# Kernel tuning notes

Measured on AMD Instinct MI355X. Metric: run time of the kernel, lower is better.

## Reference

```python
import jax, jax.numpy as jnp
import numpy as np

C_LIGHT = 1.0
CHUNK = 363  # 35937 = 99 * 363 spatial modes per scan step


def _spatial_mode_sum(r, spatial_kernel):
    # sum_n spatial_kernel[n] * sin(n * r), reduced over modes in chunks so we
    # never materialize the full [N, 35937] sin table.
    M = spatial_kernel.shape[0]
    nn = jnp.arange(M, dtype=r.dtype).reshape(-1, CHUNK)      # [steps, CHUNK]
    kk = spatial_kernel.reshape(-1, CHUNK)                    # [steps, CHUNK]

    def body(acc, nk):
        n_c, k_c = nk
        # [N, CHUNK] @ [CHUNK] -> [N]
        return acc + jnp.sin(r[:, None] * n_c[None, :]) @ k_c, None

    acc, _ = jax.lax.scan(body, jnp.zeros_like(r), (nn, kk))
    return acc


def setup_inputs() -> dict:
    key = jax.random.key(0)
    k1, k2, k3 = jax.random.split(key, 3)
    N = 131072
    M_SPATIAL = 35937   # (2*16+1)**3
    M_TEMPORAL = 33     # 2*16+1
    return {
        "spacetime_coords": jax.random.normal(k1, (N, 4), jnp.float32) * 2.0,
        "spatial_kernel": jax.random.normal(k2, (M_SPATIAL,), jnp.float32) * 0.1,
        "temporal_kernel": jax.random.normal(k3, (M_TEMPORAL,), jnp.float32) * 0.1,
        "mass_parameter": jnp.float32(1.0),
        "coupling_strength": jnp.float32(0.1),
    }


def reference(spacetime_coords, spatial_kernel, temporal_kernel,
              mass_parameter, coupling_strength):
    t = spacetime_coords[..., 0]
    x = spacetime_coords[..., 1]
    y = spacetime_coords[..., 2]
    z = spacetime_coords[..., 3]

    spatial_distance_sq = x * x + y * y + z * z
    temporal_distance_sq = (C_LIGHT * t) ** 2
    interval = temporal_distance_sq - spatial_distance_sq

    timelike = interval > 0
    lightlike = jnp.abs(interval) < 1e-10

    # Retarded Green function on the forward timelike region
    spatial_distance = jnp.sqrt(spatial_distance_sq + 1e-12)
    green = jnp.where(
        timelike & (t > 0),
        coupling_strength * jnp.exp(-mass_parameter * spatial_distance) / spatial_distance,
        jnp.zeros_like(t),
    )
    # enforce_causality mask (timelike | lightlike)
    kernel_values = jnp.where(timelike | lightlike, green, jnp.zeros_like(green))

    # Spatial component: sum_n k_n * sin(n*r) / (r + 1e-6); division factored out
    r = jnp.sqrt(spatial_distance_sq + 1e-12)
    spatial_component = _spatial_mode_sum(r, spatial_kernel) / (r + 1e-6)

    # Temporal component: sum_n k_n * cos((n+1)*0.1 * t) * exp(-0.1*|t|)
    freqs = (jnp.arange(temporal_kernel.shape[0], dtype=t.dtype) + 1.0) * 0.1
    envelope = jnp.exp(-0.1 * jnp.abs(t))
    temporal_component = (jnp.cos(t[:, None] * freqs[None, :]) @ temporal_kernel) * envelope

    total_kernel = kernel_values + spatial_component * temporal_component

    # Future light-cone causality mask
    future_lightcone = (temporal_distance_sq >= spatial_distance_sq) & (t >= 0)
    return jnp.where(future_lightcone, total_kernel, jnp.zeros_like(total_kernel))
```

## Files before the change

### kernel.cpp

```cpp
#include <hip/hip_runtime.h>
#include <math.h>


constexpr int NCHUNK = 32;

__global__ __launch_bounds__(256)
void mask_kernel(const float4* __restrict__ coords,
                 const float* __restrict__ massp,
                 const float* __restrict__ coupp,
                 const float* __restrict__ tk,
                 float* __restrict__ out,
                 int* __restrict__ counter,
                 int* __restrict__ list,
                 float* __restrict__ fw,
                 float* __restrict__ rw,
                 int N, int MT, int use_ws)
{
    int i = blockIdx.x * blockDim.x + threadIdx.x;
    if (i >= N) return;
    float4 c = coords[i];
    float t = c.x, x = c.y, y = c.z, z = c.w;
    float rsq = x * x + y * y + z * z;
    float t2  = t * t;
    bool  fl  = (t2 >= rsq) && (t >= 0.0f);
    float r   = sqrtf(rsq + 1e-12f);
    float g   = 0.0f;
    if (fl && (t2 > rsq) && (t > 0.0f))
        g = (*coupp) * expf(-(*massp) * r) / r;
    out[i] = fl ? g : 0.0f;

    if (fl && use_ws) {
        float tb = 0.1f * t;
        float T  = 0.0f;
        for (int m = 1; m <= MT; ++m)
            T = fmaf(tk[m - 1], cosf(tb * (float)m), T);
        T *= expf(-0.1f * fabsf(t));
        float f = T / (r + 1e-6f);
        int pos = atomicAdd(counter, 1);
        list[pos] = i;
        fw[pos]   = f;
        rw[pos]   = r;
    }
}

template <bool USE_LIST>
__global__ __launch_bounds__(256)
void mode_kernel(const float4* __restrict__ coords,
                 const float* __restrict__ ksp,
                 const float* __restrict__ tk,
                 float* __restrict__ out,
                 const int* __restrict__ counter,
                 const int* __restrict__ list,
                 const float* __restrict__ fw,
                 const float* __restrict__ rw,
                 int N, int M, int MT, int CH)
{
    int gtid   = blockIdx.x * blockDim.x + threadIdx.x;
    int wave   = gtid >> 6;
    int lane   = threadIdx.x & 63;
    int nwaves = (gridDim.x * blockDim.x) >> 6;

    int count = USE_LIST ? __builtin_amdgcn_readfirstlane(*counter) : N;
    int ngroups = (count + 63) >> 6;
    int items   = ngroups * NCHUNK;

    for (int it = wave; it < items; it += nwaves) {
        int group = __builtin_amdgcn_readfirstlane(it >> 5);
        int chunk = __builtin_amdgcn_readfirstlane(it & (NCHUNK - 1));
        int li    = group * 64 + lane;

        float r = 0.0f, f = 0.0f;
        int   idx = 0;
        bool  act = false;
        if (li < count) {
            if (USE_LIST) {
                idx = list[li]; r = rw[li]; f = fw[li]; act = true;
            } else {
                idx = li;
                float4 c = coords[li];
                float t = c.x;
                float rsq = c.y * c.y + c.z * c.z + c.w * c.w;
                bool fl = (t * t >= rsq) && (t >= 0.0f);
                if (fl) {
                    r = sqrtf(rsq + 1e-12f);
                    float tb = 0.1f * t;
                    float T = 0.0f;
                    for (int m = 1; m <= MT; ++m)
                        T = fmaf(tk[m - 1], cosf(tb * (float)m), T);
                    T *= expf(-0.1f * fabsf(t));
                    f = T / (r + 1e-6f);
                    act = true;
                }
            }
        }

        int n0   = chunk * CH;
        if (n0 >= M) continue;
        int n_hi = min(n0 + CH, M);

        double dr = (double)r;
        float base = (float)fmod((double)n0 * dr, 6.283185307179586);
        float t2c = 2.0f * cosf(8.0f * r);

        float sc[8], sp[8], acc[8];
#pragma unroll
        for (int j = 0; j < 8; ++j) {
            sc[j]  = sinf(fmaf((float)j,        r, base));
            sp[j]  = sinf(fmaf((float)(j - 8),  r, base));
            acc[j] = 0.0f;
        }

        const float* kc = ksp + n0;
        int len   = n_hi - n0;
        int steps = len >> 3;
        int rem   = len & 7;

        int s = 0;
        for (; s + 1 < steps; s += 2) {
            const float4 ka = *(const float4*)(kc + 8 * s);
            const float4 kb = *(const float4*)(kc + 8 * s + 4);
            const float4 kd = *(const float4*)(kc + 8 * s + 8);
            const float4 ke = *(const float4*)(kc + 8 * s + 12);
            float kv0[8] = {ka.x, ka.y, ka.z, ka.w, kb.x, kb.y, kb.z, kb.w};
            float kv1[8] = {kd.x, kd.y, kd.z, kd.w, ke.x, ke.y, ke.z, ke.w};
#pragma unroll
            for (int j = 0; j < 8; ++j) {
                acc[j] = fmaf(kv0[j], sc[j], acc[j]);
                sp[j]  = fmaf(t2c, sc[j], -sp[j]);
            }
#pragma unroll
            for (int j = 0; j < 8; ++j) {
                acc[j] = fmaf(kv1[j], sp[j], acc[j]);
                sc[j]  = fmaf(t2c, sp[j], -sc[j]);
            }
        }
        if (s < steps) {
            const float4 ka = *(const float4*)(kc + 8 * s);
            const float4 kb = *(const float4*)(kc + 8 * s + 4);
            float kv0[8] = {ka.x, ka.y, ka.z, ka.w, kb.x, kb.y, kb.z, kb.w};
#pragma unroll
            for (int j = 0; j < 8; ++j) {
                acc[j] = fmaf(kv0[j], sc[j], acc[j]);
                sp[j]  = fmaf(t2c, sc[j], -sp[j]);
            }
#pragma unroll
            for (int j = 0; j < 8; ++j) {
                float tmp = sc[j]; sc[j] = sp[j]; sp[j] = tmp;
            }
        }
        if (rem) {
#pragma unroll
            for (int j = 0; j < 8; ++j)
                if (j < rem)
                    acc[j] = fmaf(kc[8 * steps + j], sc[j], acc[j]);
        }

        float S = ((acc[0] + acc[1]) + (acc[2] + acc[3])) +
                  ((acc[4] + acc[5]) + (acc[6] + acc[7]));
        if (act)
            atomicAdd(&out[idx], S * f);
    }
}

extern "C" void kernel_launch(void* const* d_in, const int* in_sizes, int n_in,
                              void* d_out, int out_size, void* d_ws, size_t ws_size,
                              hipStream_t stream)
{
    const float4* coords = (const float4*)d_in[0];
    const float*  ksp    = (const float*)d_in[1];
    const float*  tk     = (const float*)d_in[2];
    const float*  massp  = (const float*)d_in[3];
    const float*  coupp  = (const float*)d_in[4];
    float*        out    = (float*)d_out;

    int N  = in_sizes[0] / 4;
    int M  = in_sizes[1];
    int MT = in_sizes[2];

    size_t needed = 16 + (size_t)N * 4 * 3;
    bool use_ws = (ws_size >= needed);

    int*   counter = (int*)d_ws;
    int*   list    = (int*)((char*)d_ws + 16);
    float* fw      = (float*)((char*)d_ws + 16 + (size_t)N * 4);
    float* rw      = (float*)((char*)d_ws + 16 + (size_t)N * 8);

    if (use_ws)
        hipMemsetAsync(d_ws, 0, 16, stream);

    mask_kernel<<<(N + 255) / 256, 256, 0, stream>>>(
        coords, massp, coupp, tk, out, counter, list, fw, rw, N, MT, use_ws ? 1 : 0);

    int CH = ((M + NCHUNK * 8 - 1) / (NCHUNK * 8)) * 8;

    if (use_ws)
        mode_kernel<true><<<2048, 256, 0, stream>>>(
            coords, ksp, tk, out, counter, list, fw, rw, N, M, MT, CH);
    else
        mode_kernel<false><<<2048, 256, 0, stream>>>(
            coords, ksp, tk, out, counter, list, fw, rw, N, M, MT, CH);
}
```

Measured before the change: 126.5 us.

## Pad spatial kernel, use fixed chunking, fast intrinsics, and wave-aggregated compaction

The mask kernel now copies the spatial kernel into a zero-padded workspace buffer. This lets the mode kernel run a fixed-length chunk loop with 64 chunks of 576 and no remainder handling, with the next coefficients prefetched one step ahead. The per-thread atomic used for list compaction is replaced by one ballot-based atomic per wave. Precise sin, cos and exp calls become __sinf, __cosf and __expf, and fmod becomes an rint-based range reduction, which trades accuracy for speed. The non-workspace path is replaced by a simple per-point fallback kernel.

```diff
diff --git a/kernel.cpp b/kernel.cpp
--- a/kernel.cpp
+++ b/kernel.cpp
@@ -2,127 +2,122 @@
 #include <math.h>
 
 
-constexpr int NCHUNK = 32;
+constexpr int NCHUNK = 64;
+constexpr int CH     = 576;
+constexpr int MPAD   = NCHUNK * CH + 64;
 
 __global__ __launch_bounds__(256)
 void mask_kernel(const float4* __restrict__ coords,
                  const float* __restrict__ massp,
                  const float* __restrict__ coupp,
                  const float* __restrict__ tk,
+                 const float* __restrict__ ksp,
                  float* __restrict__ out,
                  int* __restrict__ counter,
                  int* __restrict__ list,
                  float* __restrict__ fw,
                  float* __restrict__ rw,
-                 int N, int MT, int use_ws)
+                 float* __restrict__ kpad,
+                 int N, int M, int MT)
 {
     int i = blockIdx.x * blockDim.x + threadIdx.x;
+
+    if (i < MPAD) kpad[i] = (i < M) ? ksp[i] : 0.0f;
     if (i >= N) return;
+
     float4 c = coords[i];
-    float t = c.x, x = c.y, y = c.z, z = c.w;
-    float rsq = x * x + y * y + z * z;
+    float t = c.x;
+    float rsq = c.y * c.y + c.z * c.z + c.w * c.w;
     float t2  = t * t;
     bool  fl  = (t2 >= rsq) && (t >= 0.0f);
     float r   = sqrtf(rsq + 1e-12f);
     float g   = 0.0f;
     if (fl && (t2 > rsq) && (t > 0.0f))
-        g = (*coupp) * expf(-(*massp) * r) / r;
+        g = (*coupp) * __expf(-(*massp) * r) / r;
     out[i] = fl ? g : 0.0f;
 
-    if (fl && use_ws) {
+    unsigned long long bal = __ballot(fl);
+    if (fl) {
         float tb = 0.1f * t;
         float T  = 0.0f;
         for (int m = 1; m <= MT; ++m)
-            T = fmaf(tk[m - 1], cosf(tb * (float)m), T);
-        T *= expf(-0.1f * fabsf(t));
+            T = fmaf(tk[m - 1], __cosf(tb * (float)m), T);
+        T *= __expf(-0.1f * fabsf(t));
         float f = T / (r + 1e-6f);
-        int pos = atomicAdd(counter, 1);
+
+        int lane   = threadIdx.x & 63;
+        int prefix = __popcll(bal & ((1ull << lane) - 1ull));
+        int base   = 0;
+        if (prefix == 0)
+            base = atomicAdd(counter, __popcll(bal));
+        int first = __ffsll(bal) - 1;
+        base = __shfl(base, first);
+        int pos = base + prefix;
         list[pos] = i;
         fw[pos]   = f;
         rw[pos]   = r;
     }
 }
 
-template <bool USE_LIST>
 __global__ __launch_bounds__(256)
-void mode_kernel(const float4* __restrict__ coords,
-                 const float* __restrict__ ksp,
-                 const float* __restrict__ tk,
+void mode_kernel(const float* __restrict__ kpad,
                  float* __restrict__ out,
                  const int* __restrict__ counter,
                  const int* __restrict__ list,
                  const float* __restrict__ fw,
-                 const float* __restrict__ rw,
-                 int N, int M, int MT, int CH)
+                 const float* __restrict__ rw)
 {
     int gtid   = blockIdx.x * blockDim.x + threadIdx.x;
     int wave   = gtid >> 6;
     int lane   = threadIdx.x & 63;
     int nwaves = (gridDim.x * blockDim.x) >> 6;
 
-    int count = USE_LIST ? __builtin_amdgcn_readfirstlane(*counter) : N;
+    int count   = __builtin_amdgcn_readfirstlane(*counter);
     int ngroups = (count + 63) >> 6;
     int items   = ngroups * NCHUNK;
 
     for (int it = wave; it < items; it += nwaves) {
-        int group = __builtin_amdgcn_readfirstlane(it >> 5);
+        int group = __builtin_amdgcn_readfirstlane(it >> 6);
         int chunk = __builtin_amdgcn_readfirstlane(it & (NCHUNK - 1));
         int li    = group * 64 + lane;
 
+        bool  act = (li < count);
+        int   idx = 0;
         float r = 0.0f, f = 0.0f;
-        int   idx = 0;
-        bool  act = false;
-        if (li < count) {
-            if (USE_LIST) {
-                idx = list[li]; r = rw[li]; f = fw[li]; act = true;
-            } else {
-                idx = li;
-                float4 c = coords[li];
-                float t = c.x;
-                float rsq = c.y * c.y + c.z * c.z + c.w * c.w;
-                bool fl = (t * t >= rsq) && (t >= 0.0f);
-                if (fl) {
-                    r = sqrtf(rsq + 1e-12f);
-                    float tb = 0.1f * t;
-                    float T = 0.0f;
-                    for (int m = 1; m <= MT; ++m)
-                        T = fmaf(tk[m - 1], cosf(tb * (float)m), T);
-                    T *= expf(-0.1f * fabsf(t));
-                    f = T / (r + 1e-6f);
-                    act = true;
-                }
-            }
-        }
-
-        int n0   = chunk * CH;
-        if (n0 >= M) continue;
-        int n_hi = min(n0 + CH, M);
-
-        double dr = (double)r;
-        float base = (float)fmod((double)n0 * dr, 6.283185307179586);
-        float t2c = 2.0f * cosf(8.0f * r);
+        if (act) { idx = list[li]; r = rw[li]; f = fw[li]; }
+
+        int n0 = chunk * CH;
+
+        double y = (double)n0 * (double)r;
+        double q = rint(y * 0.15915494309189535);
+        float  base = (float)(y - q * 6.283185307179586);
+
+        float t2c = 2.0f * __cosf(8.0f * r);
 
         float sc[8], sp[8], acc[8];
 #pragma unroll
         for (int j = 0; j < 8; ++j) {
-            sc[j]  = sinf(fmaf((float)j,        r, base));
-            sp[j]  = sinf(fmaf((float)(j - 8),  r, base));
+            sc[j]  = __sinf(fmaf((float)j,       r, base));
+            sp[j]  = __sinf(fmaf((float)(j - 8), r, base));
             acc[j] = 0.0f;
         }
 
-        const float* kc = ksp + n0;
-        int len   = n_hi - n0;
-        int steps = len >> 3;
-        int rem   = len & 7;
-
-        int s = 0;
-        for (; s + 1 < steps; s += 2) {
-            const float4 ka = *(const float4*)(kc + 8 * s);
-            const float4 kb = *(const float4*)(kc + 8 * s + 4);
-            const float4 kd = *(const float4*)(kc + 8 * s + 8);
-            const float4 ke = *(const float4*)(kc + 8 * s + 12);
-            float kv0[8] = {ka.x, ka.y, ka.z, ka.w, kb.x, kb.y, kb.z, kb.w};
-            float kv1[8] = {kd.x, kd.y, kd.z, kd.w, ke.x, ke.y, ke.z, ke.w};
+        const float* kc = kpad + n0;
+        float4 cA = *(const float4*)(kc);
+        float4 cB = *(const float4*)(kc + 4);
+        float4 cC = *(const float4*)(kc + 8);
+        float4 cD = *(const float4*)(kc + 12);
+
+        constexpr int DSTEPS = CH / 16;
+        for (int s = 0; s < DSTEPS; ++s) {
+            const float* kn = kc + 16 * (s + 1);
+            float4 nA = *(const float4*)(kn);
+            float4 nB = *(const float4*)(kn + 4);
+            float4 nC = *(const float4*)(kn + 8);
+            float4 nD = *(const float4*)(kn + 12);
+
+            float kv0[8] = {cA.x, cA.y, cA.z, cA.w, cB.x, cB.y, cB.z, cB.w};
+            float kv1[8] = {cC.x, cC.y, cC.z, cC.w, cD.x, cD.y, cD.z, cD.w};
 #pragma unroll
             for (int j = 0; j < 8; ++j) {
                 acc[j] = fmaf(kv0[j], sc[j], acc[j]);
@@ -133,26 +128,7 @@
                 acc[j] = fmaf(kv1[j], sp[j], acc[j]);
                 sc[j]  = fmaf(t2c, sp[j], -sc[j]);
             }
-        }
-        if (s < steps) {
-            const float4 ka = *(const float4*)(kc + 8 * s);
-            const float4 kb = *(const float4*)(kc + 8 * s + 4);
-            float kv0[8] = {ka.x, ka.y, ka.z, ka.w, kb.x, kb.y, kb.z, kb.w};
-#pragma unroll
-            for (int j = 0; j < 8; ++j) {
-                acc[j] = fmaf(kv0[j], sc[j], acc[j]);
-                sp[j]  = fmaf(t2c, sc[j], -sp[j]);
-            }
-#pragma unroll
-            for (int j = 0; j < 8; ++j) {
-                float tmp = sc[j]; sc[j] = sp[j]; sp[j] = tmp;
-            }
-        }
-        if (rem) {
-#pragma unroll
-            for (int j = 0; j < 8; ++j)
-                if (j < rem)
-                    acc[j] = fmaf(kc[8 * steps + j], sc[j], acc[j]);
+            cA = nA; cB = nB; cC = nC; cD = nD;
         }
 
         float S = ((acc[0] + acc[1]) + (acc[2] + acc[3])) +
@@ -160,6 +136,46 @@
         if (act)
             atomicAdd(&out[idx], S * f);
     }
+}
+
+__global__ __launch_bounds__(256)
+void fallback_kernel(const float4* __restrict__ coords,
+                     const float* __restrict__ ksp,
+                     const float* __restrict__ tk,
+                     const float* __restrict__ massp,
+                     const float* __restrict__ coupp,
+                     float* __restrict__ out, int N, int M, int MT)
+{
+    int i = blockIdx.x * blockDim.x + threadIdx.x;
+    if (i >= N) return;
+    float4 c = coords[i];
+    float t = c.x;
+    float rsq = c.y * c.y + c.z * c.z + c.w * c.w;
+    float t2 = t * t;
+    bool fl = (t2 >= rsq) && (t >= 0.0f);
+    if (!fl) { out[i] = 0.0f; return; }
+    float r = sqrtf(rsq + 1e-12f);
+    float g = 0.0f;
+    if ((t2 > rsq) && (t > 0.0f)) g = (*coupp) * __expf(-(*massp) * r) / r;
+    float T = 0.0f, tb = 0.1f * t;
+    for (int m = 1; m <= MT; ++m) T = fmaf(tk[m - 1], __cosf(tb * (float)m), T);
+    T *= __expf(-0.1f * fabsf(t));
+    float f = T / (r + 1e-6f);
+    float S = 0.0f;
+    for (int n0 = 0; n0 < M; n0 += 1024) {
+        int nh = min(n0 + 1024, M);
+        double y = (double)n0 * (double)r;
+        double q = rint(y * 0.15915494309189535);
+        float base = (float)(y - q * 6.283185307179586);
+        float s0 = __sinf(base - r), s1 = __sinf(base);
+        float tc = 2.0f * __cosf(r);
+        for (int n = n0; n < nh; ++n) {
+            S = fmaf(ksp[n], s1, S);
+            float nx = fmaf(tc, s1, -s0);
+            s0 = s1; s1 = nx;
+        }
+    }
+    out[i] = g + S * f;
 }
 
 extern "C" void kernel_launch(void* const* d_in, const int* in_sizes, int n_in,
@@ -177,26 +193,29 @@
     int M  = in_sizes[1];
     int MT = in_sizes[2];
 
-    size_t needed = 16 + (size_t)N * 4 * 3;
-    bool use_ws = (ws_size >= needed);
+    size_t off_list = 16;
+    size_t off_fw   = off_list + (size_t)N * 4;
+    size_t off_rw   = off_fw   + (size_t)N * 4;
+    size_t off_k    = off_rw   + (size_t)N * 4;
+    size_t needed   = off_k    + (size_t)MPAD * 4;
+
+    if (ws_size < needed || M > NCHUNK * CH) {
+        fallback_kernel<<<(N + 255) / 256, 256, 0, stream>>>(
+            coords, ksp, tk, massp, coupp, out, N, M, MT);
+        return;
+    }
 
     int*   counter = (int*)d_ws;
-    int*   list    = (int*)((char*)d_ws + 16);
-    float* fw      = (float*)((char*)d_ws + 16 + (size_t)N * 4);
-    float* rw      = (float*)((char*)d_ws + 16 + (size_t)N * 8);
-
-    if (use_ws)
-        hipMemsetAsync(d_ws, 0, 16, stream);
-
-    mask_kernel<<<(N + 255) / 256, 256, 0, stream>>>(
-        coords, massp, coupp, tk, out, counter, list, fw, rw, N, MT, use_ws ? 1 : 0);
-
-    int CH = ((M + NCHUNK * 8 - 1) / (NCHUNK * 8)) * 8;
-
-    if (use_ws)
-        mode_kernel<true><<<2048, 256, 0, stream>>>(
-            coords, ksp, tk, out, counter, list, fw, rw, N, M, MT, CH);
-    else
-        mode_kernel<false><<<2048, 256, 0, stream>>>(
-            coords, ksp, tk, out, counter, list, fw, rw, N, M, MT, CH);
-}
+    int*   list    = (int*)((char*)d_ws + off_list);
+    float* fw      = (float*)((char*)d_ws + off_fw);
+    float* rw      = (float*)((char*)d_ws + off_rw);
+    float* kpad    = (float*)((char*)d_ws + off_k);
+
+    hipMemsetAsync(d_ws, 0, 16, stream);
+
+    int nthreads = (N > MPAD) ? N : MPAD;
+    mask_kernel<<<(nthreads + 255) / 256, 256, 0, stream>>>(
+        coords, massp, coupp, tk, ksp, out, counter, list, fw, rw, kpad, N, M, MT);
+
+    mode_kernel<<<2048, 256, 0, stream>>>(kpad, out, counter, list, fw, rw);
+}
```

Result: faster. 123.7 us (-2.2%).
